# Kernel optimization log

Measured on AMD Instinct MI355X. Metric: run time of the kernel, lower is better.

## Reference

```python
import jax, jax.numpy as jnp
import numpy as np

NUM_SLOTS = 24
EPS = 1e-5

def setup_inputs() -> dict:
    key = jax.random.key(0)
    k1, k2 = jax.random.split(key)
    x = jax.random.normal(k1, (4, 32, 200, 2048), dtype=jnp.float32)
    time = jax.random.randint(k2, (4, 2048), 0, NUM_SLOTS, dtype=jnp.int64)
    return {"x": x, "time": time}

def reference(x, time):
    # x: [b, c, n, t]; time: [b, t] int slot ids in [0, NUM_SLOTS)
    b, c, n, t = x.shape
    time = time[..., -t:]
    idx = time.reshape(b * t)

    # [b*t, n, c] layout matching x.permute(2,0,3,1).reshape(n, b*t, c) contraction
    xf = jnp.transpose(x, (0, 3, 2, 1)).reshape(b * t, n * c)

    # True segment-sum replaces the one-hot matmul; column L1-normalize == divide by slot count
    counts = jax.ops.segment_sum(jnp.ones((b * t,), x.dtype), idx, num_segments=NUM_SLOTS)
    denom = jnp.maximum(counts, 1e-12)[:, None]  # F.normalize eps-clamped norm

    sum_x = jax.ops.segment_sum(xf, idx, num_segments=NUM_SLOTS)            # [S, n*c]
    sum_x2 = jax.ops.segment_sum(xf * xf, idx, num_segments=NUM_SLOTS)      # [S, n*c]

    mean_slot = (sum_x / denom).reshape(NUM_SLOTS, n, c).mean(axis=1)       # [S, c]
    m2_slot = (sum_x2 / denom).reshape(NUM_SLOTS, n, c).mean(axis=1)        # [S, c]
    var_slot = m2_slot - mean_slot ** 2                                     # [S, c]

    # Embedding gather back per (b, t), broadcast over n
    sm = jnp.transpose(mean_slot[time], (0, 2, 1))[:, :, None, :]           # [b, c, 1, t]
    sv = jnp.transpose(var_slot[time], (0, 2, 1))[:, :, None, :]            # [b, c, 1, t]

    return (x - sm) / jnp.sqrt(sv + EPS)
```

## Files before the change

kernel.cpp:

```cpp
#include <hip/hip_runtime.h>
#include <math.h>

#define Bb 4
#define Cc 32
#define Nn 200
#define Tt 2048
#define Ss 24
#define EPSf 1e-5f
#define GRIDF 512

typedef float f4 __attribute__((ext_vector_type(4)));
typedef int i4 __attribute__((ext_vector_type(4)));
typedef unsigned u4 __attribute__((ext_vector_type(4)));

__device__ __forceinline__ unsigned rne_bf16(float f) {
    unsigned u = __float_as_uint(f);
    return (u + 0x7FFFu + ((u >> 16) & 1u)) >> 16;
}
__device__ __forceinline__ unsigned pack2(float a, float b) {
    return rne_bf16(a) | (rne_bf16(b) << 16);
}
__device__ __forceinline__ float lo16(unsigned u) { return __uint_as_float(u << 16); }
__device__ __forceinline__ float hi16(unsigned u) { return __uint_as_float(u & 0xFFFF0000u); }


__global__ void k_zero(int* __restrict__ counter) { *counter = 0; }

#define ROWS12(M) M(0) M(1) M(2) M(3) M(4) M(5) M(6) M(7) M(8) M(9) M(10) M(11)

#define DROW(i) u4 xb##i;

#define LROW(i) { \
    f4 v0 = *(const f4*)(bp + (size_t)(i) * Tt); \
    f4 v1 = *(const f4*)(bp + (size_t)(i) * Tt + 1024); \
    xb##i[0] = pack2(v0[0], v0[1]); \
    xb##i[1] = pack2(v0[2], v0[3]); \
    xb##i[2] = pack2(v1[0], v1[1]); \
    xb##i[3] = pack2(v1[2], v1[3]); \
    s0 += v0[0]; a0 += v0[0]*v0[0]; s1 += v0[1]; a1 += v0[1]*v0[1]; \
    s2 += v0[2]; a2 += v0[2]*v0[2]; s3 += v0[3]; a3 += v0[3]*v0[3]; \
    s4 += v1[0]; a4 += v1[0]*v1[0]; s5 += v1[1]; a5 += v1[1]*v1[1]; \
    s6 += v1[2]; a6 += v1[2]*v1[2]; s7 += v1[3]; a7 += v1[3]*v1[3]; }

#define SROW(i) { \
    f4 o0, o1; \
    o0[0] = fmaf(lo16(xb##i[0]), rr0, -mr0); \
    o0[1] = fmaf(hi16(xb##i[0]), rr1, -mr1); \
    o0[2] = fmaf(lo16(xb##i[1]), rr2, -mr2); \
    o0[3] = fmaf(hi16(xb##i[1]), rr3, -mr3); \
    o1[0] = fmaf(lo16(xb##i[2]), rr4, -mr4); \
    o1[1] = fmaf(hi16(xb##i[2]), rr5, -mr5); \
    o1[2] = fmaf(lo16(xb##i[3]), rr6, -mr6); \
    o1[3] = fmaf(hi16(xb##i[3]), rr7, -mr7); \
    __builtin_nontemporal_store(o0, (f4*)(op + (size_t)(i) * Tt)); \
    __builtin_nontemporal_store(o1, (f4*)(op + (size_t)(i) * Tt + 1024)); }

__global__ __launch_bounds__(512) void k_fuse2(const float* __restrict__ x,
                                               const int* __restrict__ timei,
                                               float2* __restrict__ part,
                                               int* __restrict__ cntp,
                                               int* __restrict__ counter,
                                               float* __restrict__ out) {
    __shared__ unsigned ldsd[7 * 4 * 512];
    __shared__ float lsum[Ss], lsq[Ss];
    __shared__ int   lcnt[Ss];
    __shared__ float s_r[Ss], s_mr[Ss];

    const int tid  = threadIdx.x;
    const int bx   = blockIdx.x;
    const int b    = bx >> 7;
    const int c    = (bx >> 2) & 31;
    const int q    = bx & 3;
    const int rg   = tid >> 8;
    const int lane = tid & 255;
    const int t0   = lane * 4;

    if (tid < Ss) { lsum[tid] = 0.f; lsq[tid] = 0.f; lcnt[tid] = 0; }
    __syncthreads();

    const i4 sl0 = *(const i4*)(timei + b * Tt + t0);
    const i4 sl1 = *(const i4*)(timei + b * Tt + t0 + 1024);

    const size_t plane = ((size_t)(b * Cc + c) * Nn + (size_t)q * 50 + (size_t)rg * 25) * Tt + t0;
    const float* bp = x + plane;

    ROWS12(DROW)
    float s0=0,s1=0,s2=0,s3=0,s4=0,s5=0,s6=0,s7=0;
    float a0=0,a1=0,a2=0,a3=0,a4=0,a5=0,a6=0,a7=0;

    ROWS12(LROW)
    for (int r = 12; r < 19; ++r) {
        f4 v0 = *(const f4*)(bp + (size_t)r * Tt);
        f4 v1 = *(const f4*)(bp + (size_t)r * Tt + 1024);
        const int base = (r - 12) * 2048 + tid;
        ldsd[base]        = pack2(v0[0], v0[1]);
        ldsd[base + 512]  = pack2(v0[2], v0[3]);
        ldsd[base + 1024] = pack2(v1[0], v1[1]);
        ldsd[base + 1536] = pack2(v1[2], v1[3]);
        s0 += v0[0]; a0 += v0[0]*v0[0]; s1 += v0[1]; a1 += v0[1]*v0[1];
        s2 += v0[2]; a2 += v0[2]*v0[2]; s3 += v0[3]; a3 += v0[3]*v0[3];
        s4 += v1[0]; a4 += v1[0]*v1[0]; s5 += v1[1]; a5 += v1[1]*v1[1];
        s6 += v1[2]; a6 += v1[2]*v1[2]; s7 += v1[3]; a7 += v1[3]*v1[3];
    }
    for (int r = 19; r < 25; ++r) {
        f4 v0 = *(const f4*)(bp + (size_t)r * Tt);
        f4 v1 = *(const f4*)(bp + (size_t)r * Tt + 1024);
        s0 += v0[0]; a0 += v0[0]*v0[0]; s1 += v0[1]; a1 += v0[1]*v0[1];
        s2 += v0[2]; a2 += v0[2]*v0[2]; s3 += v0[3]; a3 += v0[3]*v0[3];
        s4 += v1[0]; a4 += v1[0]*v1[0]; s5 += v1[1]; a5 += v1[1]*v1[1];
        s6 += v1[2]; a6 += v1[2]*v1[2]; s7 += v1[3]; a7 += v1[3]*v1[3];
    }

    atomicAdd(&lsum[sl0[0]], s0); atomicAdd(&lsq[sl0[0]], a0);
    atomicAdd(&lsum[sl0[1]], s1); atomicAdd(&lsq[sl0[1]], a1);
    atomicAdd(&lsum[sl0[2]], s2); atomicAdd(&lsq[sl0[2]], a2);
    atomicAdd(&lsum[sl0[3]], s3); atomicAdd(&lsq[sl0[3]], a3);
    atomicAdd(&lsum[sl1[0]], s4); atomicAdd(&lsq[sl1[0]], a4);
    atomicAdd(&lsum[sl1[1]], s5); atomicAdd(&lsq[sl1[1]], a5);
    atomicAdd(&lsum[sl1[2]], s6); atomicAdd(&lsq[sl1[2]], a6);
    atomicAdd(&lsum[sl1[3]], s7); atomicAdd(&lsq[sl1[3]], a7);
    if (c == 0 && q == 0 && rg == 0) {
        atomicAdd(&lcnt[sl0[0]], 1); atomicAdd(&lcnt[sl0[1]], 1);
        atomicAdd(&lcnt[sl0[2]], 1); atomicAdd(&lcnt[sl0[3]], 1);
        atomicAdd(&lcnt[sl1[0]], 1); atomicAdd(&lcnt[sl1[1]], 1);
        atomicAdd(&lcnt[sl1[2]], 1); atomicAdd(&lcnt[sl1[3]], 1);
    }
    __syncthreads();

    if (tid < Ss) {
        part[(c * Ss + tid) * 16 + (b * 4 + q)] = make_float2(lsum[tid], lsq[tid]);
        if (c == 0 && q == 0) cntp[b * Ss + tid] = lcnt[tid];
    }
    __syncthreads();

    if (tid == 0) {
        __threadfence();
        __hip_atomic_fetch_add(counter, 1, __ATOMIC_ACQ_REL, __HIP_MEMORY_SCOPE_AGENT);
        while (__hip_atomic_load(counter, __ATOMIC_ACQUIRE, __HIP_MEMORY_SCOPE_AGENT) < GRIDF)
            __builtin_amdgcn_s_sleep(2);
        __threadfence();
    }
    __syncthreads();

    if (tid < Ss) { lsum[tid] = 0.f; lsq[tid] = 0.f; }
    __syncthreads();
    if (tid < 192) {
        const int s = tid >> 3, j = tid & 7;
        float2 p0 = part[(c * Ss + s) * 16 + 2 * j];
        float2 p1 = part[(c * Ss + s) * 16 + 2 * j + 1];
        atomicAdd(&lsum[s], p0.x + p1.x);
        atomicAdd(&lsq[s],  p0.y + p1.y);
    }
    __syncthreads();
    if (tid < Ss) {
        int cnt = cntp[tid] + cntp[Ss + tid] + cntp[2 * Ss + tid] + cntp[3 * Ss + tid];
        float denom = fmaxf((float)cnt, 1e-12f) * (float)Nn;
        float m  = lsum[tid] / denom;
        float m2 = lsq[tid]  / denom;
        float rr = 1.0f / sqrtf(m2 - m * m + EPSf);
        s_r[tid]  = rr;
        s_mr[tid] = m * rr;
    }
    __syncthreads();

    const float rr0 = s_r[sl0[0]], mr0 = s_mr[sl0[0]];
    const float rr1 = s_r[sl0[1]], mr1 = s_mr[sl0[1]];
    const float rr2 = s_r[sl0[2]], mr2 = s_mr[sl0[2]];
    const float rr3 = s_r[sl0[3]], mr3 = s_mr[sl0[3]];
    const float rr4 = s_r[sl1[0]], mr4 = s_mr[sl1[0]];
    const float rr5 = s_r[sl1[1]], mr5 = s_mr[sl1[1]];
    const float rr6 = s_r[sl1[2]], mr6 = s_mr[sl1[2]];
    const float rr7 = s_r[sl1[3]], mr7 = s_mr[sl1[3]];

    float* op = out + plane;
    ROWS12(SROW)
    for (int r = 12; r < 19; ++r) {
        const int base = (r - 12) * 2048 + tid;
        const unsigned w0 = ldsd[base];
        const unsigned w1 = ldsd[base + 512];
        const unsigned w2 = ldsd[base + 1024];
        const unsigned w3 = ldsd[base + 1536];
        f4 o0, o1;
        o0[0] = fmaf(lo16(w0), rr0, -mr0);
        o0[1] = fmaf(hi16(w0), rr1, -mr1);
        o0[2] = fmaf(lo16(w1), rr2, -mr2);
        o0[3] = fmaf(hi16(w1), rr3, -mr3);
        o1[0] = fmaf(lo16(w2), rr4, -mr4);
        o1[1] = fmaf(hi16(w2), rr5, -mr5);
        o1[2] = fmaf(lo16(w3), rr6, -mr6);
        o1[3] = fmaf(hi16(w3), rr7, -mr7);
        __builtin_nontemporal_store(o0, (f4*)(op + (size_t)r * Tt));
        __builtin_nontemporal_store(o1, (f4*)(op + (size_t)r * Tt + 1024));
    }
    for (int r = 19; r < 25; ++r) {
        f4 v0 = *(const f4*)(bp + (size_t)r * Tt);
        f4 v1 = *(const f4*)(bp + (size_t)r * Tt + 1024);
        f4 o0, o1;
        o0[0] = fmaf(v0[0], rr0, -mr0);
        o0[1] = fmaf(v0[1], rr1, -mr1);
        o0[2] = fmaf(v0[2], rr2, -mr2);
        o0[3] = fmaf(v0[3], rr3, -mr3);
        o1[0] = fmaf(v1[0], rr4, -mr4);
        o1[1] = fmaf(v1[1], rr5, -mr5);
        o1[2] = fmaf(v1[2], rr6, -mr6);
        o1[3] = fmaf(v1[3], rr7, -mr7);
        __builtin_nontemporal_store(o0, (f4*)(op + (size_t)r * Tt));
        __builtin_nontemporal_store(o1, (f4*)(op + (size_t)r * Tt + 1024));
    }
}

__global__ __launch_bounds__(256) void k_stats(const float* __restrict__ x,
                                               const int* __restrict__ timei,
                                               float2* __restrict__ part,
                                               int* __restrict__ cntpart) {
    __shared__ float lsum[Ss], lsq[Ss];
    __shared__ int   lcnt[Ss];
    const int tid = threadIdx.x;
    const int bx  = blockIdx.x;
    const int tt = bx & 1;
    const int nc = (bx >> 1) & 7;
    const int bc = bx >> 4;
    const int b  = bc >> 5;
    const int c  = bc & 31;
    const bool do_hist = (c == 0 && nc == 0);

    if (tid < Ss) { lsum[tid] = 0.f; lsq[tid] = 0.f; lcnt[tid] = 0; }
    __syncthreads();

    const int t0 = tt * 1024 + tid * 4;
    const i4 sl = *(const i4*)(timei + b * Tt + t0);

    const size_t plane = ((size_t)(b * Cc + c) * Nn + (size_t)nc * 25) * Tt;
    const float* bp = x + plane + t0;

    float s0 = 0.f, s1 = 0.f, s2 = 0.f, s3 = 0.f;
    float q0 = 0.f, q1 = 0.f, q2 = 0.f, q3 = 0.f;
#pragma unroll 5
    for (int r = 0; r < 25; ++r) {
        f4 v = *(const f4*)(bp + (size_t)r * Tt);
        s0 += v[0]; q0 += v[0] * v[0];
        s1 += v[1]; q1 += v[1] * v[1];
        s2 += v[2]; q2 += v[2] * v[2];
        s3 += v[3]; q3 += v[3] * v[3];
    }

    atomicAdd(&lsum[sl[0]], s0); atomicAdd(&lsq[sl[0]], q0);
    atomicAdd(&lsum[sl[1]], s1); atomicAdd(&lsq[sl[1]], q1);
    atomicAdd(&lsum[sl[2]], s2); atomicAdd(&lsq[sl[2]], q2);
    atomicAdd(&lsum[sl[3]], s3); atomicAdd(&lsq[sl[3]], q3);
    if (do_hist) {
        atomicAdd(&lcnt[sl[0]], 1); atomicAdd(&lcnt[sl[1]], 1);
        atomicAdd(&lcnt[sl[2]], 1); atomicAdd(&lcnt[sl[3]], 1);
    }
    __syncthreads();

    const int chunk = (b * 2 + tt) * 8 + nc;
    if (tid < Ss) {
        part[(c * Ss + tid) * 64 + chunk] = make_float2(lsum[tid], lsq[tid]);
        if (do_hist) cntpart[(b * 2 + tt) * Ss + tid] = lcnt[tid];
    }
}

__global__ __launch_bounds__(256) void k_norm(const float* __restrict__ x,
                                              const int* __restrict__ timei,
                                              const float2* __restrict__ part,
                                              const int* __restrict__ cntpart,
                                              float* __restrict__ out) {
    __shared__ float lsum[Ss], lsq[Ss];
    __shared__ float s_mr[Ss], s_r[Ss];
    const int tid = threadIdx.x;
    const int bx  = blockIdx.x;
    const int b  = bx >> 7;
    const int c  = (bx >> 2) & 31;
    const int nc = bx & 3;

    if (tid < Ss) { lsum[tid] = 0.f; lsq[tid] = 0.f; }
    __syncthreads();
    if (tid < 192) {
        const int s = tid >> 3, j = tid & 7;
        const float2* pp = &part[(c * Ss + s) * 64 + j * 8];
        float ps = 0.f, pq = 0.f;
#pragma unroll
        for (int k = 0; k < 8; ++k) { ps += pp[k].x; pq += pp[k].y; }
        atomicAdd(&lsum[s], ps);
        atomicAdd(&lsq[s],  pq);
    }
    __syncthreads();
    if (tid < Ss) {
        int cnt = 0;
#pragma unroll
        for (int h = 0; h < 8; ++h) cnt += cntpart[h * Ss + tid];
        float denom = fmaxf((float)cnt, 1e-12f) * (float)Nn;
        float m  = lsum[tid] / denom;
        float m2 = lsq[tid]  / denom;
        float rr = 1.0f / sqrtf(m2 - m * m + EPSf);
        s_r[tid]  = rr;
        s_mr[tid] = m * rr;
    }
    __syncthreads();

    const int t0 = tid * 4;
    const i4 sl0 = *(const i4*)(timei + b * Tt + t0);
    const i4 sl1 = *(const i4*)(timei + b * Tt + t0 + 1024);
    const float rr0 = s_r[sl0[0]], mr0 = s_mr[sl0[0]];
    const float rr1 = s_r[sl0[1]], mr1 = s_mr[sl0[1]];
    const float rr2 = s_r[sl0[2]], mr2 = s_mr[sl0[2]];
    const float rr3 = s_r[sl0[3]], mr3 = s_mr[sl0[3]];
    const float rr4 = s_r[sl1[0]], mr4 = s_mr[sl1[0]];
    const float rr5 = s_r[sl1[1]], mr5 = s_mr[sl1[1]];
    const float rr6 = s_r[sl1[2]], mr6 = s_mr[sl1[2]];
    const float rr7 = s_r[sl1[3]], mr7 = s_mr[sl1[3]];

    const size_t plane = ((size_t)(b * Cc + c) * Nn + (size_t)nc * 50) * Tt;
    const float* xp = x + plane + t0;
    float* op = out + plane + t0;

#pragma unroll 5
    for (int r = 0; r < 50; ++r) {
        f4 v0 = *(const f4*)(xp + (size_t)r * Tt);
        f4 v1 = *(const f4*)(xp + (size_t)r * Tt + 1024);
        f4 o0, o1;
        o0[0] = fmaf(v0[0], rr0, -mr0);
        o0[1] = fmaf(v0[1], rr1, -mr1);
        o0[2] = fmaf(v0[2], rr2, -mr2);
        o0[3] = fmaf(v0[3], rr3, -mr3);
        o1[0] = fmaf(v1[0], rr4, -mr4);
        o1[1] = fmaf(v1[1], rr5, -mr5);
        o1[2] = fmaf(v1[2], rr6, -mr6);
        o1[3] = fmaf(v1[3], rr7, -mr7);
        __builtin_nontemporal_store(o0, (f4*)(op + (size_t)r * Tt));
        __builtin_nontemporal_store(o1, (f4*)(op + (size_t)r * Tt + 1024));
    }
}

extern "C" void kernel_launch(void* const* d_in, const int* in_sizes, int n_in,
                              void* d_out, int out_size, void* d_ws, size_t ws_size,
                              hipStream_t stream) {
    const float* x   = (const float*)d_in[0];
    const int* timei = (const int*)d_in[1];
    float* out = (float*)d_out;

    hipFuncAttributes fa;
    bool fused_ok = (hipFuncGetAttributes(&fa, (const void*)k_fuse2) == hipSuccess)
                    && fa.localSizeBytes == 0;
    if (fused_ok) {
        int occ = 0;
        fused_ok = (hipOccupancyMaxActiveBlocksPerMultiprocessor(&occ, k_fuse2, 512, 0)
                    == hipSuccess) && occ >= 2;
    }

    if (fused_ok) {
        float2* part = (float2*)d_ws;
        int* cntp    = (int*)((char*)d_ws + (size_t)Cc * Ss * 16 * sizeof(float2));
        int* counter = (int*)((char*)d_ws + (size_t)Cc * Ss * 16 * sizeof(float2)
                              + 128 * sizeof(int));
        k_zero<<<1, 1, 0, stream>>>(counter);
        k_fuse2<<<GRIDF, 512, 0, stream>>>(x, timei, part, cntp, counter, out);
    } else {
        float2* part = (float2*)d_ws;
        int* cnt = (int*)((char*)d_ws + (size_t)Cc * Ss * 64 * sizeof(float2));
        k_stats<<<2048, 256, 0, stream>>>(x, timei, part, cnt);
        k_norm<<<512, 256, 0, stream>>>(x, timei, part, cnt, out);
    }
}
```

Baseline: 104.0 us.

## Use 1024-thread blocks with half the grid in fused stats+normalize kernel

Restructures the fused grid-synchronized kernel from 512 blocks of 512 threads to 256 blocks of 1024 threads, each covering 100 rows of n instead of 50. This halves the number of blocks taking part in the software grid barrier and the partials per channel. The bf16 row cache in LDS drops from 7 rows to 3 rows per thread group, so more rows are re-read from global memory in the normalize phase. Partial sums are split into separate float arrays and accessed with relaxed agent-scope atomics. One block per CU must now fit for the grid barrier to stay deadlock-free.

Result: no change. 103.8 us (-0.1%).

```diff
diff --git a/kernel.cpp b/kernel.cpp
--- a/kernel.cpp
+++ b/kernel.cpp
@@ -7,7 +7,7 @@
 #define Tt 2048
 #define Ss 24
 #define EPSf 1e-5f
-#define GRIDF 512
+#define GRIDF 256
 
 typedef float f4 __attribute__((ext_vector_type(4)));
 typedef int i4 __attribute__((ext_vector_type(4)));
@@ -55,22 +55,23 @@
     __builtin_nontemporal_store(o0, (f4*)(op + (size_t)(i) * Tt)); \
     __builtin_nontemporal_store(o1, (f4*)(op + (size_t)(i) * Tt + 1024)); }
 
-__global__ __launch_bounds__(512) void k_fuse2(const float* __restrict__ x,
-                                               const int* __restrict__ timei,
-                                               float2* __restrict__ part,
-                                               int* __restrict__ cntp,
-                                               int* __restrict__ counter,
-                                               float* __restrict__ out) {
-    __shared__ unsigned ldsd[7 * 4 * 512];
+__global__ __launch_bounds__(1024) void k_fuse3(const float* __restrict__ x,
+                                                const int* __restrict__ timei,
+                                                float* __restrict__ psum,
+                                                float* __restrict__ psq,
+                                                int* __restrict__ cntp,
+                                                int* __restrict__ counter,
+                                                float* __restrict__ out) {
+    __shared__ unsigned ldsd[3 * 4096];
     __shared__ float lsum[Ss], lsq[Ss];
     __shared__ int   lcnt[Ss];
     __shared__ float s_r[Ss], s_mr[Ss];
 
     const int tid  = threadIdx.x;
     const int bx   = blockIdx.x;
-    const int b    = bx >> 7;
-    const int c    = (bx >> 2) & 31;
-    const int q    = bx & 3;
+    const int b    = bx >> 6;
+    const int c    = (bx >> 1) & 31;
+    const int h    = bx & 1;
     const int rg   = tid >> 8;
     const int lane = tid & 255;
     const int t0   = lane * 4;
@@ -81,7 +82,7 @@
     const i4 sl0 = *(const i4*)(timei + b * Tt + t0);
     const i4 sl1 = *(const i4*)(timei + b * Tt + t0 + 1024);
 
-    const size_t plane = ((size_t)(b * Cc + c) * Nn + (size_t)q * 50 + (size_t)rg * 25) * Tt + t0;
+    const size_t plane = ((size_t)(b * Cc + c) * Nn + (size_t)h * 100 + (size_t)rg * 25) * Tt + t0;
     const float* bp = x + plane;
 
     ROWS12(DROW)
@@ -89,20 +90,21 @@
     float a0=0,a1=0,a2=0,a3=0,a4=0,a5=0,a6=0,a7=0;
 
     ROWS12(LROW)
-    for (int r = 12; r < 19; ++r) {
+#pragma unroll
+    for (int r = 12; r < 15; ++r) {
         f4 v0 = *(const f4*)(bp + (size_t)r * Tt);
         f4 v1 = *(const f4*)(bp + (size_t)r * Tt + 1024);
-        const int base = (r - 12) * 2048 + tid;
+        const int base = (r - 12) * 4096 + tid;
         ldsd[base]        = pack2(v0[0], v0[1]);
-        ldsd[base + 512]  = pack2(v0[2], v0[3]);
-        ldsd[base + 1024] = pack2(v1[0], v1[1]);
-        ldsd[base + 1536] = pack2(v1[2], v1[3]);
+        ldsd[base + 1024] = pack2(v0[2], v0[3]);
+        ldsd[base + 2048] = pack2(v1[0], v1[1]);
+        ldsd[base + 3072] = pack2(v1[2], v1[3]);
         s0 += v0[0]; a0 += v0[0]*v0[0]; s1 += v0[1]; a1 += v0[1]*v0[1];
         s2 += v0[2]; a2 += v0[2]*v0[2]; s3 += v0[3]; a3 += v0[3]*v0[3];
         s4 += v1[0]; a4 += v1[0]*v1[0]; s5 += v1[1]; a5 += v1[1]*v1[1];
         s6 += v1[2]; a6 += v1[2]*v1[2]; s7 += v1[3]; a7 += v1[3]*v1[3];
     }
-    for (int r = 19; r < 25; ++r) {
+    for (int r = 15; r < 25; ++r) {
         f4 v0 = *(const f4*)(bp + (size_t)r * Tt);
         f4 v1 = *(const f4*)(bp + (size_t)r * Tt + 1024);
         s0 += v0[0]; a0 += v0[0]*v0[0]; s1 += v0[1]; a1 += v0[1]*v0[1];
@@ -119,7 +121,7 @@
     atomicAdd(&lsum[sl1[1]], s5); atomicAdd(&lsq[sl1[1]], a5);
     atomicAdd(&lsum[sl1[2]], s6); atomicAdd(&lsq[sl1[2]], a6);
     atomicAdd(&lsum[sl1[3]], s7); atomicAdd(&lsq[sl1[3]], a7);
-    if (c == 0 && q == 0 && rg == 0) {
+    if (c == 0 && h == 0 && rg == 0) {
         atomicAdd(&lcnt[sl0[0]], 1); atomicAdd(&lcnt[sl0[1]], 1);
         atomicAdd(&lcnt[sl0[2]], 1); atomicAdd(&lcnt[sl0[3]], 1);
         atomicAdd(&lcnt[sl1[0]], 1); atomicAdd(&lcnt[sl1[1]], 1);
@@ -128,8 +130,11 @@
     __syncthreads();
 
     if (tid < Ss) {
-        part[(c * Ss + tid) * 16 + (b * 4 + q)] = make_float2(lsum[tid], lsq[tid]);
-        if (c == 0 && q == 0) cntp[b * Ss + tid] = lcnt[tid];
+        const int idx = (c * Ss + tid) * 8 + (b * 2 + h);
+        __hip_atomic_store(&psum[idx], lsum[tid], __ATOMIC_RELAXED, __HIP_MEMORY_SCOPE_AGENT);
+        __hip_atomic_store(&psq[idx],  lsq[tid],  __ATOMIC_RELAXED, __HIP_MEMORY_SCOPE_AGENT);
+        if (c == 0 && h == 0)
+            __hip_atomic_store(&cntp[b * Ss + tid], lcnt[tid], __ATOMIC_RELAXED, __HIP_MEMORY_SCOPE_AGENT);
     }
     __syncthreads();
 
@@ -146,14 +151,18 @@
     __syncthreads();
     if (tid < 192) {
         const int s = tid >> 3, j = tid & 7;
-        float2 p0 = part[(c * Ss + s) * 16 + 2 * j];
-        float2 p1 = part[(c * Ss + s) * 16 + 2 * j + 1];
-        atomicAdd(&lsum[s], p0.x + p1.x);
-        atomicAdd(&lsq[s],  p0.y + p1.y);
+        const int idx = (c * Ss + s) * 8 + j;
+        float ps = __hip_atomic_load(&psum[idx], __ATOMIC_RELAXED, __HIP_MEMORY_SCOPE_AGENT);
+        float pq = __hip_atomic_load(&psq[idx],  __ATOMIC_RELAXED, __HIP_MEMORY_SCOPE_AGENT);
+        atomicAdd(&lsum[s], ps);
+        atomicAdd(&lsq[s],  pq);
     }
     __syncthreads();
     if (tid < Ss) {
-        int cnt = cntp[tid] + cntp[Ss + tid] + cntp[2 * Ss + tid] + cntp[3 * Ss + tid];
+        int cnt = 0;
+#pragma unroll
+        for (int bb = 0; bb < 4; ++bb)
+            cnt += __hip_atomic_load(&cntp[bb * Ss + tid], __ATOMIC_RELAXED, __HIP_MEMORY_SCOPE_AGENT);
         float denom = fmaxf((float)cnt, 1e-12f) * (float)Nn;
         float m  = lsum[tid] / denom;
         float m2 = lsq[tid]  / denom;
@@ -174,12 +183,13 @@
 
     float* op = out + plane;
     ROWS12(SROW)
-    for (int r = 12; r < 19; ++r) {
-        const int base = (r - 12) * 2048 + tid;
+#pragma unroll
+    for (int r = 12; r < 15; ++r) {
+        const int base = (r - 12) * 4096 + tid;
         const unsigned w0 = ldsd[base];
-        const unsigned w1 = ldsd[base + 512];
-        const unsigned w2 = ldsd[base + 1024];
-        const unsigned w3 = ldsd[base + 1536];
+        const unsigned w1 = ldsd[base + 1024];
+        const unsigned w2 = ldsd[base + 2048];
+        const unsigned w3 = ldsd[base + 3072];
         f4 o0, o1;
         o0[0] = fmaf(lo16(w0), rr0, -mr0);
         o0[1] = fmaf(hi16(w0), rr1, -mr1);
@@ -192,7 +202,7 @@
         __builtin_nontemporal_store(o0, (f4*)(op + (size_t)r * Tt));
         __builtin_nontemporal_store(o1, (f4*)(op + (size_t)r * Tt + 1024));
     }
-    for (int r = 19; r < 25; ++r) {
+    for (int r = 15; r < 25; ++r) {
         f4 v0 = *(const f4*)(bp + (size_t)r * Tt);
         f4 v1 = *(const f4*)(bp + (size_t)r * Tt + 1024);
         f4 o0, o1;
@@ -341,21 +351,22 @@
     float* out = (float*)d_out;
 
     hipFuncAttributes fa;
-    bool fused_ok = (hipFuncGetAttributes(&fa, (const void*)k_fuse2) == hipSuccess)
-                    && fa.localSizeBytes == 0;
+    bool fused_ok = (hipFuncGetAttributes(&fa, (const void*)k_fuse3) == hipSuccess)
+                    && fa.localSizeBytes == 0
+                    && fa.maxThreadsPerBlock >= 1024;
     if (fused_ok) {
         int occ = 0;
-        fused_ok = (hipOccupancyMaxActiveBlocksPerMultiprocessor(&occ, k_fuse2, 512, 0)
-                    == hipSuccess) && occ >= 2;
+        fused_ok = (hipOccupancyMaxActiveBlocksPerMultiprocessor(&occ, k_fuse3, 1024, 0)
+                    == hipSuccess) && occ >= 1;
     }
 
     if (fused_ok) {
-        float2* part = (float2*)d_ws;
-        int* cntp    = (int*)((char*)d_ws + (size_t)Cc * Ss * 16 * sizeof(float2));
-        int* counter = (int*)((char*)d_ws + (size_t)Cc * Ss * 16 * sizeof(float2)
-                              + 128 * sizeof(int));
+        float* psum  = (float*)d_ws;
+        float* psq   = psum + Cc * Ss * 8;
+        int*   cntp  = (int*)(psq + Cc * Ss * 8);
+        int*   counter = cntp + Bb * Ss + 128;
         k_zero<<<1, 1, 0, stream>>>(counter);
-        k_fuse2<<<GRIDF, 512, 0, stream>>>(x, timei, part, cntp, counter, out);
+        k_fuse3<<<GRIDF, 1024, 0, stream>>>(x, timei, psum, psq, cntp, counter, out);
     } else {
         float2* part = (float2*)d_ws;
         int* cnt = (int*)((char*)d_ws + (size_t)Cc * Ss * 64 * sizeof(float2));
```
